# Performance work log

Hardware: AMD Instinct MI355X
Metric: run time of the kernel (lower is better)

Reference implementation:

```python
import jax, jax.numpy as jnp
import numpy as np

H = 1024
NH = 16
HD = H // NH  # 64

def setup_inputs() -> dict:
    key = jax.random.key(0)
    ks = jax.random.split(key, 6)
    B, S = 2, 2048
    hidden_states = jax.random.normal(ks[0], (B, S, H), dtype=jnp.float32)
    attention_mask = jnp.ones((B, S), dtype=jnp.int32)
    sc = 1.0 / np.sqrt(H)
    Wq = jax.random.normal(ks[1], (H, H), dtype=jnp.float32) * sc
    Wk = jax.random.normal(ks[2], (H, H), dtype=jnp.float32) * sc
    Wv = jax.random.normal(ks[3], (H, H), dtype=jnp.float32) * sc
    Wo = jax.random.normal(ks[4], (H, H), dtype=jnp.float32) * sc
    return {"hidden_states": hidden_states, "attention_mask": attention_mask,
            "Wq": Wq, "Wk": Wk, "Wv": Wv, "Wo": Wo}

def reference(hidden_states, attention_mask, Wq, Wk, Wv, Wo):
    B, S, _ = hidden_states.shape
    # nn.Linear(bias=False): y = x @ W.T
    q = hidden_states @ Wq.T
    k = hidden_states @ Wk.T
    v = hidden_states @ Wv.T
    # [B, NH, S, HD]
    q = q.reshape(B, S, NH, HD).transpose(0, 2, 1, 3)
    k = k.reshape(B, S, NH, HD).transpose(0, 2, 1, 3)
    v = v.reshape(B, S, NH, HD).transpose(0, 2, 1, 3)
    # ELU+1 feature map
    q = jax.nn.elu(q) + 1.0
    k = jax.nn.elu(k) + 1.0
    # [B, NH, S, S]
    attn = jnp.einsum('bhqd,bhkd->bhqk', q, k)
    mask = attention_mask[:, None, None, :]  # [B,1,1,S]
    attn = jnp.where(mask == 0, -jnp.inf, attn)
    attn = jax.nn.softmax(attn, axis=-1)
    # dropout p=0.0 (eval) -> identity
    out = jnp.einsum('bhqk,bhkd->bhqd', attn, v)
    out = out.transpose(0, 2, 1, 3).reshape(B, S, H)
    return out @ Wo.T
```

## Files before the change

### kernel.cpp

```cpp
#include <hip/hip_runtime.h>

#define H_ 1024
#define NH_ 16
#define HD_ 64
#define B_ 2
#define S_ 2048
#define BS_ 4096

typedef _Float16 half8 __attribute__((ext_vector_type(8)));
typedef _Float16 half4_t __attribute__((ext_vector_type(4)));
typedef float floatx4 __attribute__((ext_vector_type(4)));

#define LOG2E 1.44269504088896f

__device__ __forceinline__ void async_copy16(void* lds, const void* g) {
  __builtin_amdgcn_global_load_lds(
      (const __attribute__((address_space(1))) unsigned int*)g,
      (__attribute__((address_space(3))) unsigned int*)lds, 16, 0, 0);
}

__global__ __launch_bounds__(256) void cvt_all(
    const float* __restrict__ hs, const float* __restrict__ wq,
    const float* __restrict__ wk, const float* __restrict__ wv,
    const float* __restrict__ wo,
    _Float16* __restrict__ hs_h, _Float16* __restrict__ w_h) {
  int i = blockIdx.x * 256 + threadIdx.x;
  int idx = i * 4;
  const float* src; _Float16* dst; int off;
  if (idx < BS_ * H_) {
    src = hs; dst = hs_h; off = idx;
  } else {
    int j = idx - BS_ * H_;
    int w = j >> 20;
    off = j & ((1 << 20) - 1);
    src = (w == 0) ? wq : (w == 1) ? wk : (w == 2) ? wv : wo;
    dst = w_h + (size_t)w * (H_ * H_);
  }
  float4 f = *(const float4*)(src + off);
  half4_t o;
  o.x = (_Float16)f.x; o.y = (_Float16)f.y;
  o.z = (_Float16)f.z; o.w = (_Float16)f.w;
  *(half4_t*)(dst + off) = o;
}

__global__ __launch_bounds__(256, 2) void qkv_gemm(
    const _Float16* __restrict__ A, const _Float16* __restrict__ Wall,
    _Float16* __restrict__ qh, _Float16* __restrict__ kh,
    _Float16* __restrict__ vt) {
  const int z = blockIdx.z;
  const _Float16* W = Wall + (size_t)z * (H_ * H_);
  const int rbase = blockIdx.y * 128;
  const int cbase = blockIdx.x * 64;
  __shared__ _Float16 Ab[3][128 * 64];
  __shared__ _Float16 Bb[3][64 * 64];
  const int tid = threadIdx.x, lane = tid & 63, w = tid >> 6;
  const int quad = lane >> 4, l16 = lane & 15;

  floatx4 zero = {0.f, 0.f, 0.f, 0.f};
  floatx4 acc[2][4];
#pragma unroll
  for (int i = 0; i < 2; ++i)
#pragma unroll
    for (int j = 0; j < 4; ++j) acc[i][j] = zero;

  const int srow = tid >> 3;
  const int pslot = tid & 7;
  const int sslot = pslot ^ (srow & 7);
  const _Float16* Ag = A + (size_t)(rbase + srow) * H_ + sslot * 8;
  const _Float16* Bg = W + (size_t)(cbase + srow) * H_ + sslot * 8;

  auto STAGE = [&](int s, int t) {
    const int k0 = t * 64;
    _Float16* ab = &Ab[s][tid * 8];
    _Float16* bb = &Bb[s][tid * 8];
#pragma unroll
    for (int u = 0; u < 4; ++u)
      async_copy16(ab + u * 2048, Ag + (size_t)(u * 32) * H_ + k0);
#pragma unroll
    for (int u = 0; u < 2; ++u)
      async_copy16(bb + u * 2048, Bg + (size_t)(u * 32) * H_ + k0);
  };

  const int rsw = l16 & 7;
  auto COMPUTE = [&](int s) {
    const _Float16* Ap = &Ab[s][0];
    const _Float16* Bp = &Bb[s][0];
    half8 af[2][2], bf[4][2];
#pragma unroll
    for (int i = 0; i < 2; ++i)
#pragma unroll
      for (int hh = 0; hh < 2; ++hh)
        af[i][hh] = *(const half8*)&Ap[(w * 32 + i * 16 + l16) * 64 +
                                       (((hh * 4 + quad) ^ rsw) * 8)];
#pragma unroll
    for (int j = 0; j < 4; ++j)
#pragma unroll
      for (int hh = 0; hh < 2; ++hh)
        bf[j][hh] = *(const half8*)&Bp[(j * 16 + l16) * 64 +
                                       (((hh * 4 + quad) ^ rsw) * 8)];
    __builtin_amdgcn_s_setprio(1);
#pragma unroll
    for (int i = 0; i < 2; ++i)
#pragma unroll
      for (int j = 0; j < 4; ++j) {
        acc[i][j] = __builtin_amdgcn_mfma_f32_16x16x32_f16(af[i][0], bf[j][0],
                                                           acc[i][j], 0, 0, 0);
        acc[i][j] = __builtin_amdgcn_mfma_f32_16x16x32_f16(af[i][1], bf[j][1],
                                                           acc[i][j], 0, 0, 0);
      }
    __builtin_amdgcn_s_setprio(0);
  };

  STAGE(0, 0);
  STAGE(1, 1);
  int sc = 0;
  for (int t = 0; t < 14; ++t) {
    asm volatile("s_waitcnt vmcnt(6)" ::: "memory");
    __builtin_amdgcn_sched_barrier(0);
    __builtin_amdgcn_s_barrier();
    __builtin_amdgcn_sched_barrier(0);
    int ss = sc + 2; if (ss >= 3) ss -= 3;
    STAGE(ss, t + 2);
    COMPUTE(sc);
    sc = (sc == 2) ? 0 : sc + 1;
  }
  asm volatile("s_waitcnt vmcnt(6)" ::: "memory");
  __builtin_amdgcn_sched_barrier(0);
  __builtin_amdgcn_s_barrier();
  __builtin_amdgcn_sched_barrier(0);
  COMPUTE(sc);
  sc = (sc == 2) ? 0 : sc + 1;
  asm volatile("s_waitcnt vmcnt(0)" ::: "memory");
  __builtin_amdgcn_sched_barrier(0);
  __builtin_amdgcn_s_barrier();
  __builtin_amdgcn_sched_barrier(0);
  COMPUTE(sc);

#pragma unroll
  for (int i = 0; i < 2; ++i) {
    int r0 = rbase + w * 32 + i * 16 + quad * 4;
    int b = r0 >> 11, sl0 = r0 & (S_ - 1);
#pragma unroll
    for (int j = 0; j < 4; ++j) {
      int col = cbase + j * 16 + l16;
      int h = col >> 6, d = col & 63;
      if (z == 2) {
        half4_t pk;
#pragma unroll
        for (int r = 0; r < 4; ++r) pk[r] = (_Float16)acc[i][j][r];
        *(half4_t*)&vt[((size_t)(b * NH_ + h) * HD_ + d) * S_ + sl0] = pk;
      } else {
        _Float16* outp = (z == 0) ? qh : kh;
        float scale = (z == 0) ? LOG2E : 1.0f;
#pragma unroll
        for (int r = 0; r < 4; ++r) {
          float x = acc[i][j][r];
          x = ((x > 0.f) ? (x + 1.f) : __expf(x)) * scale;
          outp[((size_t)(b * NH_ + h) * S_ + sl0 + r) * HD_ + d] = (_Float16)x;
        }
      }
    }
  }
}

__global__ __launch_bounds__(256, 2) void flash_attn(
    const _Float16* __restrict__ qh, const _Float16* __restrict__ kh,
    const _Float16* __restrict__ vt, const int* __restrict__ mask,
    _Float16* __restrict__ attn_out) {
  const int bh = blockIdx.y, b = bh >> 4, h = bh & 15;
  const int qbase = blockIdx.x * 128;
  const int tid = threadIdx.x, w = tid >> 6, lane = tid & 63;
  const int quad = lane >> 4, l16 = lane & 15;

  __shared__ _Float16 Kt[2][128 * 64];
  __shared__ _Float16 Vt[2][64 * 128];

  const _Float16* Q = qh + (size_t)bh * (S_ * HD_);
  const _Float16* K = kh + (size_t)bh * (S_ * HD_);
  const _Float16* Vg = vt + (size_t)bh * (HD_ * S_);
  const int* Mb = mask + b * S_;

  half8 qf[2][2];
#pragma unroll
  for (int g = 0; g < 2; ++g) {
    int qr = qbase + w * 32 + g * 16 + l16;
    qf[g][0] = *(const half8*)&Q[qr * 64 + quad * 8];
    qf[g][1] = *(const half8*)&Q[qr * 64 + 32 + quad * 8];
  }

  floatx4 zero = {0.f, 0.f, 0.f, 0.f};
  floatx4 o[2][4];
#pragma unroll
  for (int g = 0; g < 2; ++g)
#pragma unroll
    for (int i = 0; i < 4; ++i) o[g][i] = zero;
  float mi[2] = {-3e38f, -3e38f}, li[2] = {0.f, 0.f};

  const int krow_off = lane >> 3;
  const int kslot = lane & 7;
  const int kchunk = kslot ^ (krow_off & 7);
  const int vrow_off = lane >> 4;
  const int vslot = lane & 15;

  {
#pragma unroll
    for (int u = 0; u < 4; ++u) {
      int kl = w * 32 + u * 8;
      async_copy16(&Kt[0][kl * 64], K + (size_t)(kl + krow_off) * 64 + kchunk * 8);
    }
#pragma unroll
    for (int u = 0; u < 4; ++u) {
      int d0 = w * 16 + u * 4 + vrow_off;
      int c0 = vslot ^ (d0 & 15);
      async_copy16(&Vt[0][(w * 16 + u * 4) * 128], Vg + (size_t)d0 * S_ + c0 * 8);
    }
  }

  for (int kt = 0; kt < S_ / 128; ++kt) {
    const int key0 = kt * 128;
    const int buf = kt & 1;
    __syncthreads();
    if (kt < S_ / 128 - 1) {
      const int key1 = key0 + 128;
#pragma unroll
      for (int u = 0; u < 4; ++u) {
        int kl = w * 32 + u * 8;
        async_copy16(&Kt[buf ^ 1][kl * 64],
                     K + (size_t)(key1 + kl + krow_off) * 64 + kchunk * 8);
      }
#pragma unroll
      for (int u = 0; u < 4; ++u) {
        int d0 = w * 16 + u * 4 + vrow_off;
        int c0 = vslot ^ (d0 & 15);
        async_copy16(&Vt[buf ^ 1][(w * 16 + u * 4) * 128],
                     Vg + (size_t)d0 * S_ + key1 + c0 * 8);
      }
    }
    int m0 = Mb[key0 + lane];
    int m1 = Mb[key0 + 64 + lane];

    const _Float16* Kb = &Kt[buf][0];
    const _Float16* Vb = &Vt[buf][0];

    floatx4 sa[2][8];
#pragma unroll
    for (int g = 0; g < 2; ++g)
#pragma unroll
      for (int ct = 0; ct < 8; ++ct) sa[g][ct] = zero;
    {
      int s0 = quad ^ (l16 & 7);
      int s1 = (4 + quad) ^ (l16 & 7);
#pragma unroll
      for (int ct = 0; ct < 8; ++ct) {
        int key = ct * 16 + l16;
        half8 bf0 = *(half8*)&Kb[key * 64 + s0 * 8];
        half8 bf1 = *(half8*)&Kb[key * 64 + s1 * 8];
        sa[0][ct] = __builtin_amdgcn_mfma_f32_16x16x32_f16(bf0, qf[0][0], sa[0][ct], 0, 0, 0);
        sa[0][ct] = __builtin_amdgcn_mfma_f32_16x16x32_f16(bf1, qf[0][1], sa[0][ct], 0, 0, 0);
        sa[1][ct] = __builtin_amdgcn_mfma_f32_16x16x32_f16(bf0, qf[1][0], sa[1][ct], 0, 0, 0);
        sa[1][ct] = __builtin_amdgcn_mfma_f32_16x16x32_f16(bf1, qf[1][1], sa[1][ct], 0, 0, 0);
      }
    }
    if (__any((m0 == 0) || (m1 == 0))) {
#pragma unroll
      for (int ct = 0; ct < 8; ++ct)
#pragma unroll
        for (int r = 0; r < 4; ++r)
          if (Mb[key0 + ct * 16 + quad * 4 + r] == 0) {
            sa[0][ct][r] = -1e30f;
            sa[1][ct][r] = -1e30f;
          }
    }
#pragma unroll
    for (int g = 0; g < 2; ++g) {
      float mx = sa[g][0][0];
#pragma unroll
      for (int ct = 0; ct < 8; ++ct)
#pragma unroll
        for (int r = 0; r < 4; ++r) mx = fmaxf(mx, sa[g][ct][r]);
      mx = fmaxf(mx, __shfl_xor(mx, 16));
      mx = fmaxf(mx, __shfl_xor(mx, 32));
      float mn = fmaxf(mi[g], mx);
      float alpha = __builtin_amdgcn_exp2f(mi[g] - mn);
      mi[g] = mn;
      float rs = 0.f;
#pragma unroll
      for (int ct = 0; ct < 8; ++ct)
#pragma unroll
        for (int r = 0; r < 4; ++r) {
          float p = __builtin_amdgcn_exp2f(sa[g][ct][r] - mn);
          sa[g][ct][r] = p;
          rs += p;
        }
      rs += __shfl_xor(rs, 16);
      rs += __shfl_xor(rs, 32);
      li[g] = li[g] * alpha + rs;
#pragma unroll
      for (int ct2 = 0; ct2 < 4; ++ct2) {
        o[g][ct2][0] *= alpha; o[g][ct2][1] *= alpha;
        o[g][ct2][2] *= alpha; o[g][ct2][3] *= alpha;
      }
    }
#pragma unroll
    for (int ct = 0; ct < 8; ++ct) {
      half4_t p0, p1;
#pragma unroll
      for (int r = 0; r < 4; ++r) {
        p0[r] = (_Float16)sa[0][ct][r];
        p1[r] = (_Float16)sa[1][ct][r];
      }
      int chunk = (2 * ct + (quad >> 1)) ^ l16;
      int off = chunk * 8 + (quad & 1) * 4;
#pragma unroll
      for (int ct2 = 0; ct2 < 4; ++ct2) {
        int d = ct2 * 16 + l16;
        half4_t vf = *(half4_t*)&Vb[d * 128 + off];
        o[0][ct2] = __builtin_amdgcn_mfma_f32_16x16x16f16(vf, p0, o[0][ct2], 0, 0, 0);
        o[1][ct2] = __builtin_amdgcn_mfma_f32_16x16x16f16(vf, p1, o[1][ct2], 0, 0, 0);
      }
    }
  }
#pragma unroll
  for (int g = 0; g < 2; ++g) {
    float inv = 1.0f / li[g];
    int row = qbase + w * 32 + g * 16 + l16;
#pragma unroll
    for (int ct2 = 0; ct2 < 4; ++ct2) {
      half4_t pk;
#pragma unroll
      for (int r = 0; r < 4; ++r) pk[r] = (_Float16)(o[g][ct2][r] * inv);
      int d = ct2 * 16 + quad * 4;
      *(half4_t*)&attn_out[((size_t)(b * S_ + row)) * H_ + h * HD_ + d] = pk;
    }
  }
}

__global__ __launch_bounds__(256, 2) void out_gemm(
    const _Float16* __restrict__ A, const _Float16* __restrict__ W,
    float* __restrict__ out) {
  const int rbase = blockIdx.y * 128;
  const int cbase = blockIdx.x * 64;
  __shared__ _Float16 Ab[3][128 * 64];
  __shared__ _Float16 Bb[3][64 * 64];
  const int tid = threadIdx.x, lane = tid & 63, w = tid >> 6;
  const int quad = lane >> 4, l16 = lane & 15;

  floatx4 zero = {0.f, 0.f, 0.f, 0.f};
  floatx4 acc[2][4];
#pragma unroll
  for (int i = 0; i < 2; ++i)
#pragma unroll
    for (int j = 0; j < 4; ++j) acc[i][j] = zero;

  const int srow = tid >> 3;
  const int pslot = tid & 7;
  const int sslot = pslot ^ (srow & 7);
  const _Float16* Ag = A + (size_t)(rbase + srow) * H_ + sslot * 8;
  const _Float16* Bg = W + (size_t)(cbase + srow) * H_ + sslot * 8;

  auto STAGE = [&](int s, int t) {
    const int k0 = t * 64;
    _Float16* ab = &Ab[s][tid * 8];
    _Float16* bb = &Bb[s][tid * 8];
#pragma unroll
    for (int u = 0; u < 4; ++u)
      async_copy16(ab + u * 2048, Ag + (size_t)(u * 32) * H_ + k0);
#pragma unroll
    for (int u = 0; u < 2; ++u)
      async_copy16(bb + u * 2048, Bg + (size_t)(u * 32) * H_ + k0);
  };

  const int rsw = l16 & 7;
  auto COMPUTE = [&](int s) {
    const _Float16* Ap = &Ab[s][0];
    const _Float16* Bp = &Bb[s][0];
    half8 af[2][2], bf[4][2];
#pragma unroll
    for (int i = 0; i < 2; ++i)
#pragma unroll
      for (int hh = 0; hh < 2; ++hh)
        af[i][hh] = *(const half8*)&Ap[(w * 32 + i * 16 + l16) * 64 +
                                       (((hh * 4 + quad) ^ rsw) * 8)];
#pragma unroll
    for (int j = 0; j < 4; ++j)
#pragma unroll
      for (int hh = 0; hh < 2; ++hh)
        bf[j][hh] = *(const half8*)&Bp[(j * 16 + l16) * 64 +
                                       (((hh * 4 + quad) ^ rsw) * 8)];
    __builtin_amdgcn_s_setprio(1);
#pragma unroll
    for (int i = 0; i < 2; ++i)
#pragma unroll
      for (int j = 0; j < 4; ++j) {
        acc[i][j] = __builtin_amdgcn_mfma_f32_16x16x32_f16(af[i][0], bf[j][0],
                                                           acc[i][j], 0, 0, 0);
        acc[i][j] = __builtin_amdgcn_mfma_f32_16x16x32_f16(af[i][1], bf[j][1],
                                                           acc[i][j], 0, 0, 0);
      }
    __builtin_amdgcn_s_setprio(0);
  };

  STAGE(0, 0);
  STAGE(1, 1);
  int sc = 0;
  for (int t = 0; t < 14; ++t) {
    asm volatile("s_waitcnt vmcnt(6)" ::: "memory");
    __builtin_amdgcn_sched_barrier(0);
    __builtin_amdgcn_s_barrier();
    __builtin_amdgcn_sched_barrier(0);
    int ss = sc + 2; if (ss >= 3) ss -= 3;
    STAGE(ss, t + 2);
    COMPUTE(sc);
    sc = (sc == 2) ? 0 : sc + 1;
  }
  asm volatile("s_waitcnt vmcnt(6)" ::: "memory");
  __builtin_amdgcn_sched_barrier(0);
  __builtin_amdgcn_s_barrier();
  __builtin_amdgcn_sched_barrier(0);
  COMPUTE(sc);
  sc = (sc == 2) ? 0 : sc + 1;
  asm volatile("s_waitcnt vmcnt(0)" ::: "memory");
  __builtin_amdgcn_sched_barrier(0);
  __builtin_amdgcn_s_barrier();
  __builtin_amdgcn_sched_barrier(0);
  COMPUTE(sc);

#pragma unroll
  for (int i = 0; i < 2; ++i) {
    int r0 = rbase + w * 32 + i * 16 + quad * 4;
#pragma unroll
    for (int j = 0; j < 4; ++j) {
      int col = cbase + j * 16 + l16;
#pragma unroll
      for (int r = 0; r < 4; ++r)
        out[(size_t)(r0 + r) * H_ + col] = acc[i][j][r];
    }
  }
}

extern "C" void kernel_launch(void* const* d_in, const int* in_sizes, int n_in,
                              void* d_out, int out_size, void* d_ws,
                              size_t ws_size, hipStream_t stream) {
  const float* hs = (const float*)d_in[0];
  const int* mask = (const int*)d_in[1];
  const float* Wq = (const float*)d_in[2];
  const float* Wk = (const float*)d_in[3];
  const float* Wv = (const float*)d_in[4];
  const float* Wo = (const float*)d_in[5];
  float* out = (float*)d_out;

  _Float16* p = (_Float16*)d_ws;
  _Float16* hs_h = p; p += (size_t)BS_ * H_;
  _Float16* w_h = p;  p += (size_t)4 * H_ * H_;
  _Float16* q_h = p;  p += (size_t)BS_ * H_;
  _Float16* k_h = p;  p += (size_t)BS_ * H_;
  _Float16* v_t = p;  p += (size_t)BS_ * H_;
  _Float16* ao_h = p; p += (size_t)BS_ * H_;

  cvt_all<<<8192, 256, 0, stream>>>(hs, Wq, Wk, Wv, Wo, hs_h, w_h);
  qkv_gemm<<<dim3(16, 32, 3), 256, 0, stream>>>(hs_h, w_h, q_h, k_h, v_t);
  flash_attn<<<dim3(16, 32), 256, 0, stream>>>(q_h, k_h, v_t, mask, ao_h);
  out_gemm<<<dim3(16, 32), 256, 0, stream>>>(ao_h, w_h + (size_t)3 * H_ * H_, out);
}
```

Measured before the change: 201.0 us.

## Enlarge QKV GEMM tile to 128x128 with 2x2 warp layout and double buffering

The QKV projection GEMM now uses 128x128 output tiles per block, with each of four warps computing a 64x64 sub-tile, so the grid is halved in x. It also replaces the triple-buffered pipeline (explicit vmcnt waits and s_barrier) with a simpler double-buffered loop synchronized by __syncthreads. The larger tile raises arithmetic intensity and LDS/register reuse per fragment load. In exchange it uses more accumulator registers, yields fewer blocks (768), and has a shallower prefetch depth that may expose load latency.

```diff
diff --git a/kernel.cpp b/kernel.cpp
--- a/kernel.cpp
+++ b/kernel.cpp
@@ -50,6 +50,278 @@
   const int z = blockIdx.z;
   const _Float16* W = Wall + (size_t)z * (H_ * H_);
   const int rbase = blockIdx.y * 128;
+  const int cbase = blockIdx.x * 128;
+  __shared__ _Float16 Ab[2][128 * 64];
+  __shared__ _Float16 Bb[2][128 * 64];
+  const int tid = threadIdx.x, lane = tid & 63, w = tid >> 6;
+  const int quad = lane >> 4, l16 = lane & 15;
+  const int wr = (w >> 1) * 64, wc = (w & 1) * 64;
+
+  floatx4 zero = {0.f, 0.f, 0.f, 0.f};
+  floatx4 acc[4][4];
+#pragma unroll
+  for (int i = 0; i < 4; ++i)
+#pragma unroll
+    for (int j = 0; j < 4; ++j) acc[i][j] = zero;
+
+  const int srow = tid >> 3;
+  const int pslot = tid & 7;
+  const int sslot = pslot ^ (srow & 7);
+  const _Float16* Ag = A + (size_t)(rbase + srow) * H_ + sslot * 8;
+  const _Float16* Bg = W + (size_t)(cbase + srow) * H_ + sslot * 8;
+
+  auto STAGE = [&](int s, int t) {
+    const int k0 = t * 64;
+    _Float16* ab = &Ab[s][tid * 8];
+    _Float16* bb = &Bb[s][tid * 8];
+#pragma unroll
+    for (int u = 0; u < 4; ++u)
+      async_copy16(ab + u * 2048, Ag + (size_t)(u * 32) * H_ + k0);
+#pragma unroll
+    for (int u = 0; u < 4; ++u)
+      async_copy16(bb + u * 2048, Bg + (size_t)(u * 32) * H_ + k0);
+  };
+
+  const int rsw = l16 & 7;
+  auto COMPUTE = [&](int s) {
+    const _Float16* Ap = &Ab[s][0];
+    const _Float16* Bp = &Bb[s][0];
+    half8 af[4][2], bf[4][2];
+#pragma unroll
+    for (int t = 0; t < 4; ++t)
+#pragma unroll
+      for (int hh = 0; hh < 2; ++hh)
+        af[t][hh] = *(const half8*)&Ap[(wr + t * 16 + l16) * 64 +
+                                       (((hh * 4 + quad) ^ rsw) * 8)];
+#pragma unroll
+    for (int t = 0; t < 4; ++t)
+#pragma unroll
+      for (int hh = 0; hh < 2; ++hh)
+        bf[t][hh] = *(const half8*)&Bp[(wc + t * 16 + l16) * 64 +
+                                       (((hh * 4 + quad) ^ rsw) * 8)];
+    __builtin_amdgcn_s_setprio(1);
+#pragma unroll
+    for (int i = 0; i < 4; ++i)
+#pragma unroll
+      for (int j = 0; j < 4; ++j) {
+        acc[i][j] = __builtin_amdgcn_mfma_f32_16x16x32_f16(af[i][0], bf[j][0],
+                                                           acc[i][j], 0, 0, 0);
+        acc[i][j] = __builtin_amdgcn_mfma_f32_16x16x32_f16(af[i][1], bf[j][1],
+                                                           acc[i][j], 0, 0, 0);
+      }
+    __builtin_amdgcn_s_setprio(0);
+  };
+
+  STAGE(0, 0);
+  for (int t = 0; t < 16; ++t) {
+    __syncthreads();
+    if (t < 15) STAGE((t + 1) & 1, t + 1);
+    COMPUTE(t & 1);
+  }
+
+#pragma unroll
+  for (int i = 0; i < 4; ++i) {
+    int r0 = rbase + wr + i * 16 + quad * 4;
+    int b = r0 >> 11, sl0 = r0 & (S_ - 1);
+#pragma unroll
+    for (int j = 0; j < 4; ++j) {
+      int col = cbase + wc + j * 16 + l16;
+      int h = col >> 6, d = col & 63;
+      if (z == 2) {
+        half4_t pk;
+#pragma unroll
+        for (int r = 0; r < 4; ++r) pk[r] = (_Float16)acc[i][j][r];
+        *(half4_t*)&vt[((size_t)(b * NH_ + h) * HD_ + d) * S_ + sl0] = pk;
+      } else {
+        _Float16* outp = (z == 0) ? qh : kh;
+        float scale = (z == 0) ? LOG2E : 1.0f;
+#pragma unroll
+        for (int r = 0; r < 4; ++r) {
+          float x = acc[i][j][r];
+          x = ((x > 0.f) ? (x + 1.f) : __expf(x)) * scale;
+          outp[((size_t)(b * NH_ + h) * S_ + sl0 + r) * HD_ + d] = (_Float16)x;
+        }
+      }
+    }
+  }
+}
+
+__global__ __launch_bounds__(256, 2) void flash_attn(
+    const _Float16* __restrict__ qh, const _Float16* __restrict__ kh,
+    const _Float16* __restrict__ vt, const int* __restrict__ mask,
+    _Float16* __restrict__ attn_out) {
+  const int bh = blockIdx.y, b = bh >> 4, h = bh & 15;
+  const int qbase = blockIdx.x * 128;
+  const int tid = threadIdx.x, w = tid >> 6, lane = tid & 63;
+  const int quad = lane >> 4, l16 = lane & 15;
+
+  __shared__ _Float16 Kt[2][128 * 64];
+  __shared__ _Float16 Vt[2][64 * 128];
+
+  const _Float16* Q = qh + (size_t)bh * (S_ * HD_);
+  const _Float16* K = kh + (size_t)bh * (S_ * HD_);
+  const _Float16* Vg = vt + (size_t)bh * (HD_ * S_);
+  const int* Mb = mask + b * S_;
+
+  half8 qf[2][2];
+#pragma unroll
+  for (int g = 0; g < 2; ++g) {
+    int qr = qbase + w * 32 + g * 16 + l16;
+    qf[g][0] = *(const half8*)&Q[qr * 64 + quad * 8];
+    qf[g][1] = *(const half8*)&Q[qr * 64 + 32 + quad * 8];
+  }
+
+  floatx4 zero = {0.f, 0.f, 0.f, 0.f};
+  floatx4 o[2][4];
+#pragma unroll
+  for (int g = 0; g < 2; ++g)
+#pragma unroll
+    for (int i = 0; i < 4; ++i) o[g][i] = zero;
+  float mi[2] = {-3e38f, -3e38f}, li[2] = {0.f, 0.f};
+
+  const int krow_off = lane >> 3;
+  const int kslot = lane & 7;
+  const int kchunk = kslot ^ (krow_off & 7);
+  const int vrow_off = lane >> 4;
+  const int vslot = lane & 15;
+
+  {
+#pragma unroll
+    for (int u = 0; u < 4; ++u) {
+      int kl = w * 32 + u * 8;
+      async_copy16(&Kt[0][kl * 64], K + (size_t)(kl + krow_off) * 64 + kchunk * 8);
+    }
+#pragma unroll
+    for (int u = 0; u < 4; ++u) {
+      int d0 = w * 16 + u * 4 + vrow_off;
+      int c0 = vslot ^ (d0 & 15);
+      async_copy16(&Vt[0][(w * 16 + u * 4) * 128], Vg + (size_t)d0 * S_ + c0 * 8);
+    }
+  }
+
+  for (int kt = 0; kt < S_ / 128; ++kt) {
+    const int key0 = kt * 128;
+    const int buf = kt & 1;
+    __syncthreads();
+    if (kt < S_ / 128 - 1) {
+      const int key1 = key0 + 128;
+#pragma unroll
+      for (int u = 0; u < 4; ++u) {
+        int kl = w * 32 + u * 8;
+        async_copy16(&Kt[buf ^ 1][kl * 64],
+                     K + (size_t)(key1 + kl + krow_off) * 64 + kchunk * 8);
+      }
+#pragma unroll
+      for (int u = 0; u < 4; ++u) {
+        int d0 = w * 16 + u * 4 + vrow_off;
+        int c0 = vslot ^ (d0 & 15);
+        async_copy16(&Vt[buf ^ 1][(w * 16 + u * 4) * 128],
+                     Vg + (size_t)d0 * S_ + key1 + c0 * 8);
+      }
+    }
+    int m0 = Mb[key0 + lane];
+    int m1 = Mb[key0 + 64 + lane];
+
+    const _Float16* Kb = &Kt[buf][0];
+    const _Float16* Vb = &Vt[buf][0];
+
+    floatx4 sa[2][8];
+#pragma unroll
+    for (int g = 0; g < 2; ++g)
+#pragma unroll
+      for (int ct = 0; ct < 8; ++ct) sa[g][ct] = zero;
+    {
+      int s0 = quad ^ (l16 & 7);
+      int s1 = (4 + quad) ^ (l16 & 7);
+#pragma unroll
+      for (int ct = 0; ct < 8; ++ct) {
+        int key = ct * 16 + l16;
+        half8 bf0 = *(half8*)&Kb[key * 64 + s0 * 8];
+        half8 bf1 = *(half8*)&Kb[key * 64 + s1 * 8];
+        sa[0][ct] = __builtin_amdgcn_mfma_f32_16x16x32_f16(bf0, qf[0][0], sa[0][ct], 0, 0, 0);
+        sa[0][ct] = __builtin_amdgcn_mfma_f32_16x16x32_f16(bf1, qf[0][1], sa[0][ct], 0, 0, 0);
+        sa[1][ct] = __builtin_amdgcn_mfma_f32_16x16x32_f16(bf0, qf[1][0], sa[1][ct], 0, 0, 0);
+        sa[1][ct] = __builtin_amdgcn_mfma_f32_16x16x32_f16(bf1, qf[1][1], sa[1][ct], 0, 0, 0);
+      }
+    }
+    if (__any((m0 == 0) || (m1 == 0))) {
+#pragma unroll
+      for (int ct = 0; ct < 8; ++ct)
+#pragma unroll
+        for (int r = 0; r < 4; ++r)
+          if (Mb[key0 + ct * 16 + quad * 4 + r] == 0) {
+            sa[0][ct][r] = -1e30f;
+            sa[1][ct][r] = -1e30f;
+          }
+    }
+#pragma unroll
+    for (int g = 0; g < 2; ++g) {
+      float mx = sa[g][0][0];
+#pragma unroll
+      for (int ct = 0; ct < 8; ++ct)
+#pragma unroll
+        for (int r = 0; r < 4; ++r) mx = fmaxf(mx, sa[g][ct][r]);
+      mx = fmaxf(mx, __shfl_xor(mx, 16));
+      mx = fmaxf(mx, __shfl_xor(mx, 32));
+      float mn = fmaxf(mi[g], mx);
+      float alpha = __builtin_amdgcn_exp2f(mi[g] - mn);
+      mi[g] = mn;
+      float rs = 0.f;
+#pragma unroll
+      for (int ct = 0; ct < 8; ++ct)
+#pragma unroll
+        for (int r = 0; r < 4; ++r) {
+          float p = __builtin_amdgcn_exp2f(sa[g][ct][r] - mn);
+          sa[g][ct][r] = p;
+          rs += p;
+        }
+      rs += __shfl_xor(rs, 16);
+      rs += __shfl_xor(rs, 32);
+      li[g] = li[g] * alpha + rs;
+#pragma unroll
+      for (int ct2 = 0; ct2 < 4; ++ct2) {
+        o[g][ct2][0] *= alpha; o[g][ct2][1] *= alpha;
+        o[g][ct2][2] *= alpha; o[g][ct2][3] *= alpha;
+      }
+    }
+#pragma unroll
+    for (int ct = 0; ct < 8; ++ct) {
+      half4_t p0, p1;
+#pragma unroll
+      for (int r = 0; r < 4; ++r) {
+        p0[r] = (_Float16)sa[0][ct][r];
+        p1[r] = (_Float16)sa[1][ct][r];
+      }
+      int chunk = (2 * ct + (quad >> 1)) ^ l16;
+      int off = chunk * 8 + (quad & 1) * 4;
+#pragma unroll
+      for (int ct2 = 0; ct2 < 4; ++ct2) {
+        int d = ct2 * 16 + l16;
+        half4_t vf = *(half4_t*)&Vb[d * 128 + off];
+        o[0][ct2] = __builtin_amdgcn_mfma_f32_16x16x16f16(vf, p0, o[0][ct2], 0, 0, 0);
+        o[1][ct2] = __builtin_amdgcn_mfma_f32_16x16x16f16(vf, p1, o[1][ct2], 0, 0, 0);
+      }
+    }
+  }
+#pragma unroll
+  for (int g = 0; g < 2; ++g) {
+    float inv = 1.0f / li[g];
+    int row = qbase + w * 32 + g * 16 + l16;
+#pragma unroll
+    for (int ct2 = 0; ct2 < 4; ++ct2) {
+      half4_t pk;
+#pragma unroll
+      for (int r = 0; r < 4; ++r) pk[r] = (_Float16)(o[g][ct2][r] * inv);
+      int d = ct2 * 16 + quad * 4;
+      *(half4_t*)&attn_out[((size_t)(b * S_ + row)) * H_ + h * HD_ + d] = pk;
+    }
+  }
+}
+
+__global__ __launch_bounds__(256, 2) void out_gemm(
+    const _Float16* __restrict__ A, const _Float16* __restrict__ W,
+    float* __restrict__ out) {
+  const int rbase = blockIdx.y * 128;
   const int cbase = blockIdx.x * 64;
   __shared__ _Float16 Ab[3][128 * 64];
   __shared__ _Float16 Bb[3][64 * 64];
@@ -139,295 +411,6 @@
 #pragma unroll
   for (int i = 0; i < 2; ++i) {
     int r0 = rbase + w * 32 + i * 16 + quad * 4;
-    int b = r0 >> 11, sl0 = r0 & (S_ - 1);
-#pragma unroll
-    for (int j = 0; j < 4; ++j) {
-      int col = cbase + j * 16 + l16;
-      int h = col >> 6, d = col & 63;
-      if (z == 2) {
-        half4_t pk;
-#pragma unroll
-        for (int r = 0; r < 4; ++r) pk[r] = (_Float16)acc[i][j][r];
-        *(half4_t*)&vt[((size_t)(b * NH_ + h) * HD_ + d) * S_ + sl0] = pk;
-      } else {
-        _Float16* outp = (z == 0) ? qh : kh;
-        float scale = (z == 0) ? LOG2E : 1.0f;
-#pragma unroll
-        for (int r = 0; r < 4; ++r) {
-          float x = acc[i][j][r];
-          x = ((x > 0.f) ? (x + 1.f) : __expf(x)) * scale;
-          outp[((size_t)(b * NH_ + h) * S_ + sl0 + r) * HD_ + d] = (_Float16)x;
-        }
-      }
-    }
-  }
-}
-
-__global__ __launch_bounds__(256, 2) void flash_attn(
-    const _Float16* __restrict__ qh, const _Float16* __restrict__ kh,
-    const _Float16* __restrict__ vt, const int* __restrict__ mask,
-    _Float16* __restrict__ attn_out) {
-  const int bh = blockIdx.y, b = bh >> 4, h = bh & 15;
-  const int qbase = blockIdx.x * 128;
-  const int tid = threadIdx.x, w = tid >> 6, lane = tid & 63;
-  const int quad = lane >> 4, l16 = lane & 15;
-
-  __shared__ _Float16 Kt[2][128 * 64];
-  __shared__ _Float16 Vt[2][64 * 128];
-
-  const _Float16* Q = qh + (size_t)bh * (S_ * HD_);
-  const _Float16* K = kh + (size_t)bh * (S_ * HD_);
-  const _Float16* Vg = vt + (size_t)bh * (HD_ * S_);
-  const int* Mb = mask + b * S_;
-
-  half8 qf[2][2];
-#pragma unroll
-  for (int g = 0; g < 2; ++g) {
-    int qr = qbase + w * 32 + g * 16 + l16;
-    qf[g][0] = *(const half8*)&Q[qr * 64 + quad * 8];
-    qf[g][1] = *(const half8*)&Q[qr * 64 + 32 + quad * 8];
-  }
-
-  floatx4 zero = {0.f, 0.f, 0.f, 0.f};
-  floatx4 o[2][4];
-#pragma unroll
-  for (int g = 0; g < 2; ++g)
-#pragma unroll
-    for (int i = 0; i < 4; ++i) o[g][i] = zero;
-  float mi[2] = {-3e38f, -3e38f}, li[2] = {0.f, 0.f};
-
-  const int krow_off = lane >> 3;
-  const int kslot = lane & 7;
-  const int kchunk = kslot ^ (krow_off & 7);
-  const int vrow_off = lane >> 4;
-  const int vslot = lane & 15;
-
-  {
-#pragma unroll
-    for (int u = 0; u < 4; ++u) {
-      int kl = w * 32 + u * 8;
-      async_copy16(&Kt[0][kl * 64], K + (size_t)(kl + krow_off) * 64 + kchunk * 8);
-    }
-#pragma unroll
-    for (int u = 0; u < 4; ++u) {
-      int d0 = w * 16 + u * 4 + vrow_off;
-      int c0 = vslot ^ (d0 & 15);
-      async_copy16(&Vt[0][(w * 16 + u * 4) * 128], Vg + (size_t)d0 * S_ + c0 * 8);
-    }
-  }
-
-  for (int kt = 0; kt < S_ / 128; ++kt) {
-    const int key0 = kt * 128;
-    const int buf = kt & 1;
-    __syncthreads();
-    if (kt < S_ / 128 - 1) {
-      const int key1 = key0 + 128;
-#pragma unroll
-      for (int u = 0; u < 4; ++u) {
-        int kl = w * 32 + u * 8;
-        async_copy16(&Kt[buf ^ 1][kl * 64],
-                     K + (size_t)(key1 + kl + krow_off) * 64 + kchunk * 8);
-      }
-#pragma unroll
-      for (int u = 0; u < 4; ++u) {
-        int d0 = w * 16 + u * 4 + vrow_off;
-        int c0 = vslot ^ (d0 & 15);
-        async_copy16(&Vt[buf ^ 1][(w * 16 + u * 4) * 128],
-                     Vg + (size_t)d0 * S_ + key1 + c0 * 8);
-      }
-    }
-    int m0 = Mb[key0 + lane];
-    int m1 = Mb[key0 + 64 + lane];
-
-    const _Float16* Kb = &Kt[buf][0];
-    const _Float16* Vb = &Vt[buf][0];
-
-    floatx4 sa[2][8];
-#pragma unroll
-    for (int g = 0; g < 2; ++g)
-#pragma unroll
-      for (int ct = 0; ct < 8; ++ct) sa[g][ct] = zero;
-    {
-      int s0 = quad ^ (l16 & 7);
-      int s1 = (4 + quad) ^ (l16 & 7);
-#pragma unroll
-      for (int ct = 0; ct < 8; ++ct) {
-        int key = ct * 16 + l16;
-        half8 bf0 = *(half8*)&Kb[key * 64 + s0 * 8];
-        half8 bf1 = *(half8*)&Kb[key * 64 + s1 * 8];
-        sa[0][ct] = __builtin_amdgcn_mfma_f32_16x16x32_f16(bf0, qf[0][0], sa[0][ct], 0, 0, 0);
-        sa[0][ct] = __builtin_amdgcn_mfma_f32_16x16x32_f16(bf1, qf[0][1], sa[0][ct], 0, 0, 0);
-        sa[1][ct] = __builtin_amdgcn_mfma_f32_16x16x32_f16(bf0, qf[1][0], sa[1][ct], 0, 0, 0);
-        sa[1][ct] = __builtin_amdgcn_mfma_f32_16x16x32_f16(bf1, qf[1][1], sa[1][ct], 0, 0, 0);
-      }
-    }
-    if (__any((m0 == 0) || (m1 == 0))) {
-#pragma unroll
-      for (int ct = 0; ct < 8; ++ct)
-#pragma unroll
-        for (int r = 0; r < 4; ++r)
-          if (Mb[key0 + ct * 16 + quad * 4 + r] == 0) {
-            sa[0][ct][r] = -1e30f;
-            sa[1][ct][r] = -1e30f;
-          }
-    }
-#pragma unroll
-    for (int g = 0; g < 2; ++g) {
-      float mx = sa[g][0][0];
-#pragma unroll
-      for (int ct = 0; ct < 8; ++ct)
-#pragma unroll
-        for (int r = 0; r < 4; ++r) mx = fmaxf(mx, sa[g][ct][r]);
-      mx = fmaxf(mx, __shfl_xor(mx, 16));
-      mx = fmaxf(mx, __shfl_xor(mx, 32));
-      float mn = fmaxf(mi[g], mx);
-      float alpha = __builtin_amdgcn_exp2f(mi[g] - mn);
-      mi[g] = mn;
-      float rs = 0.f;
-#pragma unroll
-      for (int ct = 0; ct < 8; ++ct)
-#pragma unroll
-        for (int r = 0; r < 4; ++r) {
-          float p = __builtin_amdgcn_exp2f(sa[g][ct][r] - mn);
-          sa[g][ct][r] = p;
-          rs += p;
-        }
-      rs += __shfl_xor(rs, 16);
-      rs += __shfl_xor(rs, 32);
-      li[g] = li[g] * alpha + rs;
-#pragma unroll
-      for (int ct2 = 0; ct2 < 4; ++ct2) {
-        o[g][ct2][0] *= alpha; o[g][ct2][1] *= alpha;
-        o[g][ct2][2] *= alpha; o[g][ct2][3] *= alpha;
-      }
-    }
-#pragma unroll
-    for (int ct = 0; ct < 8; ++ct) {
-      half4_t p0, p1;
-#pragma unroll
-      for (int r = 0; r < 4; ++r) {
-        p0[r] = (_Float16)sa[0][ct][r];
-        p1[r] = (_Float16)sa[1][ct][r];
-      }
-      int chunk = (2 * ct + (quad >> 1)) ^ l16;
-      int off = chunk * 8 + (quad & 1) * 4;
-#pragma unroll
-      for (int ct2 = 0; ct2 < 4; ++ct2) {
-        int d = ct2 * 16 + l16;
-        half4_t vf = *(half4_t*)&Vb[d * 128 + off];
-        o[0][ct2] = __builtin_amdgcn_mfma_f32_16x16x16f16(vf, p0, o[0][ct2], 0, 0, 0);
-        o[1][ct2] = __builtin_amdgcn_mfma_f32_16x16x16f16(vf, p1, o[1][ct2], 0, 0, 0);
-      }
-    }
-  }
-#pragma unroll
-  for (int g = 0; g < 2; ++g) {
-    float inv = 1.0f / li[g];
-    int row = qbase + w * 32 + g * 16 + l16;
-#pragma unroll
-    for (int ct2 = 0; ct2 < 4; ++ct2) {
-      half4_t pk;
-#pragma unroll
-      for (int r = 0; r < 4; ++r) pk[r] = (_Float16)(o[g][ct2][r] * inv);
-      int d = ct2 * 16 + quad * 4;
-      *(half4_t*)&attn_out[((size_t)(b * S_ + row)) * H_ + h * HD_ + d] = pk;
-    }
-  }
-}
-
-__global__ __launch_bounds__(256, 2) void out_gemm(
-    const _Float16* __restrict__ A, const _Float16* __restrict__ W,
-    float* __restrict__ out) {
-  const int rbase = blockIdx.y * 128;
-  const int cbase = blockIdx.x * 64;
-  __shared__ _Float16 Ab[3][128 * 64];
-  __shared__ _Float16 Bb[3][64 * 64];
-  const int tid = threadIdx.x, lane = tid & 63, w = tid >> 6;
-  const int quad = lane >> 4, l16 = lane & 15;
-
-  floatx4 zero = {0.f, 0.f, 0.f, 0.f};
-  floatx4 acc[2][4];
-#pragma unroll
-  for (int i = 0; i < 2; ++i)
-#pragma unroll
-    for (int j = 0; j < 4; ++j) acc[i][j] = zero;
-
-  const int srow = tid >> 3;
-  const int pslot = tid & 7;
-  const int sslot = pslot ^ (srow & 7);
-  const _Float16* Ag = A + (size_t)(rbase + srow) * H_ + sslot * 8;
-  const _Float16* Bg = W + (size_t)(cbase + srow) * H_ + sslot * 8;
-
-  auto STAGE = [&](int s, int t) {
-    const int k0 = t * 64;
-    _Float16* ab = &Ab[s][tid * 8];
-    _Float16* bb = &Bb[s][tid * 8];
-#pragma unroll
-    for (int u = 0; u < 4; ++u)
-      async_copy16(ab + u * 2048, Ag + (size_t)(u * 32) * H_ + k0);
-#pragma unroll
-    for (int u = 0; u < 2; ++u)
-      async_copy16(bb + u * 2048, Bg + (size_t)(u * 32) * H_ + k0);
-  };
-
-  const int rsw = l16 & 7;
-  auto COMPUTE = [&](int s) {
-    const _Float16* Ap = &Ab[s][0];
-    const _Float16* Bp = &Bb[s][0];
-    half8 af[2][2], bf[4][2];
-#pragma unroll
-    for (int i = 0; i < 2; ++i)
-#pragma unroll
-      for (int hh = 0; hh < 2; ++hh)
-        af[i][hh] = *(const half8*)&Ap[(w * 32 + i * 16 + l16) * 64 +
-                                       (((hh * 4 + quad) ^ rsw) * 8)];
-#pragma unroll
-    for (int j = 0; j < 4; ++j)
-#pragma unroll
-      for (int hh = 0; hh < 2; ++hh)
-        bf[j][hh] = *(const half8*)&Bp[(j * 16 + l16) * 64 +
-                                       (((hh * 4 + quad) ^ rsw) * 8)];
-    __builtin_amdgcn_s_setprio(1);
-#pragma unroll
-    for (int i = 0; i < 2; ++i)
-#pragma unroll
-      for (int j = 0; j < 4; ++j) {
-        acc[i][j] = __builtin_amdgcn_mfma_f32_16x16x32_f16(af[i][0], bf[j][0],
-                                                           acc[i][j], 0, 0, 0);
-        acc[i][j] = __builtin_amdgcn_mfma_f32_16x16x32_f16(af[i][1], bf[j][1],
-                                                           acc[i][j], 0, 0, 0);
-      }
-    __builtin_amdgcn_s_setprio(0);
-  };
-
-  STAGE(0, 0);
-  STAGE(1, 1);
-  int sc = 0;
-  for (int t = 0; t < 14; ++t) {
-    asm volatile("s_waitcnt vmcnt(6)" ::: "memory");
-    __builtin_amdgcn_sched_barrier(0);
-    __builtin_amdgcn_s_barrier();
-    __builtin_amdgcn_sched_barrier(0);
-    int ss = sc + 2; if (ss >= 3) ss -= 3;
-    STAGE(ss, t + 2);
-    COMPUTE(sc);
-    sc = (sc == 2) ? 0 : sc + 1;
-  }
-  asm volatile("s_waitcnt vmcnt(6)" ::: "memory");
-  __builtin_amdgcn_sched_barrier(0);
-  __builtin_amdgcn_s_barrier();
-  __builtin_amdgcn_sched_barrier(0);
-  COMPUTE(sc);
-  sc = (sc == 2) ? 0 : sc + 1;
-  asm volatile("s_waitcnt vmcnt(0)" ::: "memory");
-  __builtin_amdgcn_sched_barrier(0);
-  __builtin_amdgcn_s_barrier();
-  __builtin_amdgcn_sched_barrier(0);
-  COMPUTE(sc);
-
-#pragma unroll
-  for (int i = 0; i < 2; ++i) {
-    int r0 = rbase + w * 32 + i * 16 + quad * 4;
 #pragma unroll
     for (int j = 0; j < 4; ++j) {
       int col = cbase + j * 16 + l16;
@@ -458,7 +441,7 @@
   _Float16* ao_h = p; p += (size_t)BS_ * H_;
 
   cvt_all<<<8192, 256, 0, stream>>>(hs, Wq, Wk, Wv, Wo, hs_h, w_h);
-  qkv_gemm<<<dim3(16, 32, 3), 256, 0, stream>>>(hs_h, w_h, q_h, k_h, v_t);
+  qkv_gemm<<<dim3(8, 32, 3), 256, 0, stream>>>(hs_h, w_h, q_h, k_h, v_t);
   flash_attn<<<dim3(16, 32), 256, 0, stream>>>(q_h, k_h, v_t, mask, ao_h);
   out_gemm<<<dim3(16, 32), 256, 0, stream>>>(ao_h, w_h + (size_t)3 * H_ * H_, out);
 }
```

New measurement: 202.5 us. Within noise of the previous version (+0.7%).
